# Optimization experiments

Hardware: AMD Instinct MI355X
Metric: run time of the kernel (lower is better)

## Reference

```python
import jax, jax.numpy as jnp
import numpy as np

EPS = 1e-08


def setup_inputs() -> dict:
    key = jax.random.key(0)
    x = jax.random.normal(key, (64, 16, 65536), dtype=jnp.float32)
    return {"x": x}


def reference(x):
    # x: (B, C, T). All statistics reduce over the last (time) axis.
    mean = x.mean(axis=-1)                       # (B, C)
    var = jnp.var(x, axis=-1, ddof=1)            # torch.var default: unbiased
    std = jnp.sqrt(var)                          # torch.std default: unbiased
    sq_mean = (x ** 2).mean(axis=-1)
    rms = jnp.sqrt(sq_mean)
    peak = x.max(axis=-1)
    peak_neg = x.min(axis=-1)
    peak_to_peak = peak - peak_neg
    abs_peak = jnp.abs(peak)
    crest_factor = abs_peak / (rms + EPS)
    mean_abs = jnp.abs(x).mean(axis=-1)
    shape_factor = rms / (mean_abs + EPS)
    impulse_factor = abs_peak / (mean_abs + EPS)
    sqrt_mean = jnp.sqrt(jnp.abs(x)).mean(axis=-1)
    clearance_factor = abs_peak / (sqrt_mean ** 2 + EPS)

    centered = x - mean[..., None]               # (B, C, T)
    skewness = (centered ** 3).mean(axis=-1) / (std ** 3 + EPS)
    kurtosis_val = (centered ** 4).mean(axis=-1) / (std ** 4 + EPS) - 3.0

    signs = jnp.sign(x)
    zcr = (signs[:, :, 1:] != signs[:, :, :-1]).astype(jnp.float32).mean(axis=-1)
    centered_signs = jnp.sign(centered)
    mcr = (centered_signs[:, :, 1:] != centered_signs[:, :, :-1]).astype(jnp.float32).mean(axis=-1)

    margin_factor = abs_peak / (sqrt_mean + EPS)
    energy = (x ** 2).sum(axis=-1)

    features = jnp.stack([
        mean, std, var, rms, peak, peak_neg, peak_to_peak,
        crest_factor, shape_factor, impulse_factor, clearance_factor,
        skewness, kurtosis_val, zcr, mcr, margin_factor, energy,
    ], axis=-1)                                  # (B, C, 17)
    return features
```

## Files before the change

### kernel.cpp

```cpp
#include <hip/hip_runtime.h>
#include <math.h>

#define T_LEN  65536
#define TPB    256
#define VECS   (T_LEN / 4)
#define VPT    (VECS / TPB)
#define NSUPER (VPT / 4)
#define NWAVES (TPB / 64)
#define NB     (VECS / 64)
#define EPS    1e-8f

#define BANDB  0.05f
#define WCAP   1536

struct Acc {
    float s1, s2, s3, s4, sa, ss, mx, mn;
    int mcb;
};

__device__ __forceinline__ int mbcnt64(unsigned long long m) {
    int c = __builtin_amdgcn_mbcnt_lo((unsigned)m, 0);
    return __builtin_amdgcn_mbcnt_hi((unsigned)(m >> 32), c);
}

__device__ __forceinline__ void pair_cls(float p, float q, Acc& a,
                                         float2* __restrict__ mycand, int& wcnt) {
    float lo = fminf(p, q), hi = fmaxf(p, q);
    bool always = (lo < -BANDB) && (hi >= BANDB);
    bool never  = (lo >= BANDB) || (hi < -BANDB);
    a.mcb += (int)always;
    bool st = !(always || never);
    unsigned long long mask = __ballot(st);
    if (st) {
        int o = wcnt + mbcnt64(mask);
        if (o < WCAP) mycand[o] = make_float2(lo, hi);
    }
    wcnt += __builtin_popcountll(mask);
}

__device__ __forceinline__ void p1_body(const float4& v, int lane, Acc& a,
                                        float2* __restrict__ mycand, int& wcnt) {
    float prev = __shfl_up(v.w, 1);
    if (lane == 0) prev = v.x;

    pair_cls(prev, v.x, a, mycand, wcnt);
    pair_cls(v.x, v.y, a, mycand, wcnt);
    pair_cls(v.y, v.z, a, mycand, wcnt);
    pair_cls(v.z, v.w, a, mycand, wcnt);

    float e0 = v.x, e1 = v.y, e2 = v.z, e3 = v.w;
    a.s1 += e0 + e1 + e2 + e3;
    a.s2 = fmaf(e0, e0, a.s2); a.s2 = fmaf(e1, e1, a.s2);
    a.s2 = fmaf(e2, e2, a.s2); a.s2 = fmaf(e3, e3, a.s2);
    a.s3 = fmaf(e0 * e0, e0, a.s3); a.s3 = fmaf(e1 * e1, e1, a.s3);
    a.s3 = fmaf(e2 * e2, e2, a.s3); a.s3 = fmaf(e3 * e3, e3, a.s3);
    a.s4 = fmaf(e0 * e0, e0 * e0, a.s4); a.s4 = fmaf(e1 * e1, e1 * e1, a.s4);
    a.s4 = fmaf(e2 * e2, e2 * e2, a.s4); a.s4 = fmaf(e3 * e3, e3 * e3, a.s4);
    float a0 = fabsf(e0), a1 = fabsf(e1), a2 = fabsf(e2), a3 = fabsf(e3);
    a.sa += a0 + a1 + a2 + a3;
    a.ss += __builtin_amdgcn_sqrtf(a0) + __builtin_amdgcn_sqrtf(a1)
          + __builtin_amdgcn_sqrtf(a2) + __builtin_amdgcn_sqrtf(a3);
    a.mx = fmaxf(fmaxf(a.mx, e0), fmaxf(e1, fmaxf(e2, e3)));
    a.mn = fminf(fminf(a.mn, e0), fminf(e1, fminf(e2, e3)));
}

__device__ __forceinline__ void p2f(const float4& v, int lane, float m,
                                    int& mc, int& zc) {
    float prev = __shfl_up(v.w, 1);
    if (lane == 0) prev = v.x;
    bool spm = prev < m, szp = prev < 0.f;
    bool m0 = v.x < m, m1 = v.y < m, m2 = v.z < m, m3 = v.w < m;
    bool z0 = v.x < 0.f, z1 = v.y < 0.f, z2 = v.z < 0.f, z3 = v.w < 0.f;
    mc += (int)(spm != m0) + (int)(m0 != m1) + (int)(m1 != m2) + (int)(m2 != m3);
    zc += (int)(szp != z0) + (int)(z0 != z1) + (int)(z1 != z2) + (int)(z2 != z3);
}

__global__ __launch_bounds__(TPB) void stat_feat_fused(const float* __restrict__ x,
                                                       float* __restrict__ out) {
    const int row  = blockIdx.x;
    const int tid  = threadIdx.x;
    const int lane = tid & 63;
    const int wave = tid >> 6;

    const float4* __restrict__ xv = (const float4*)(x + (size_t)row * T_LEN);

    __shared__ float  l[10][NWAVES];
    __shared__ float  s_mean;
    __shared__ float  wlast[NB];
    __shared__ float  xfirst[NB];
    __shared__ float2 cand[NWAVES * WCAP];
    __shared__ int    wc[NWAVES];

    float2* __restrict__ mycand = cand + wave * WCAP;
    int wcnt = 0;

    Acc a;
    a.s1 = a.s2 = a.s3 = a.s4 = a.sa = a.ss = 0.f;
    a.mx = -__builtin_inff();
    a.mn = __builtin_inff();
    a.mcb = 0;

    for (int g = 0; g < NSUPER; ++g) {
        const int base = g * 4 * TPB + tid;
        const int ia = base, ib = base + TPB, ic = base + 2 * TPB, id = base + 3 * TPB;
        float4 va = xv[ia];
        float4 vb = xv[ib];
        float4 vc = xv[ic];
        float4 vd = xv[id];
        if (lane == 63) {
            wlast[ia >> 6] = va.w; wlast[ib >> 6] = vb.w;
            wlast[ic >> 6] = vc.w; wlast[id >> 6] = vd.w;
        }
        if (lane == 0) {
            xfirst[ia >> 6] = va.x; xfirst[ib >> 6] = vb.x;
            xfirst[ic >> 6] = vc.x; xfirst[id >> 6] = vd.x;
        }
        p1_body(va, lane, a, mycand, wcnt);
        p1_body(vb, lane, a, mycand, wcnt);
        p1_body(vc, lane, a, mycand, wcnt);
        p1_body(vd, lane, a, mycand, wcnt);
    }

#pragma unroll
    for (int o = 32; o > 0; o >>= 1) {
        a.s1 += __shfl_down(a.s1, o);
        a.s2 += __shfl_down(a.s2, o);
        a.s3 += __shfl_down(a.s3, o);
        a.s4 += __shfl_down(a.s4, o);
        a.sa += __shfl_down(a.sa, o);
        a.ss += __shfl_down(a.ss, o);
        a.mcb += __shfl_down(a.mcb, o);
        a.mx = fmaxf(a.mx, __shfl_down(a.mx, o));
        a.mn = fminf(a.mn, __shfl_down(a.mn, o));
    }

    if (lane == 0) {
        l[0][wave] = a.s1; l[1][wave] = a.s2; l[2][wave] = a.s3; l[3][wave] = a.s4;
        l[4][wave] = a.sa; l[5][wave] = a.ss; l[6][wave] = a.mx; l[7][wave] = a.mn;
        l[8][wave] = (float)a.mcb;
        wc[wave] = wcnt;
    }
    __syncthreads();

    float S1 = 0.f, S2 = 0.f, S3 = 0.f, S4 = 0.f, SA = 0.f, SS = 0.f, MCB = 0.f;
    float MX = -__builtin_inff(), MN = __builtin_inff();
    if (tid == 0) {
#pragma unroll
        for (int wv = 0; wv < NWAVES; wv++) {
            S1 += l[0][wv]; S2 += l[1][wv]; S3 += l[2][wv]; S4 += l[3][wv];
            SA += l[4][wv]; SS += l[5][wv];
            MX = fmaxf(MX, l[6][wv]); MN = fminf(MN, l[7][wv]);
            MCB += l[8][wv];
        }
        s_mean = S1 / (float)T_LEN;
    }
    __syncthreads();

    const float m = s_mean;
    const bool fb = (fabsf(m) >= BANDB) | (wc[0] > WCAP) | (wc[1] > WCAP)
                  | (wc[2] > WCAP) | (wc[3] > WCAP);
    int mcc = 0, zcc = 0;
    if (!fb) {
#pragma unroll
        for (int w = 0; w < NWAVES; w++) {
            const int n = wc[w];
            const float2* __restrict__ cw = cand + w * WCAP;
            for (int i = tid; i < n; i += TPB) {
                float2 c = cw[i];
                mcc += (int)((c.x < m) && (c.y >= m));
                zcc += (int)((c.x < 0.f) && (c.y >= 0.f));
            }
        }
    } else {
        for (int g = 0; g < NSUPER; ++g) {
            const int base = g * 4 * TPB + tid;
            const int ia = base, ib = base + TPB, ic = base + 2 * TPB, id = base + 3 * TPB;
            float4 va = xv[ia];
            float4 vb = xv[ib];
            float4 vc = xv[ic];
            float4 vd = xv[id];
            p2f(va, lane, m, mcc, zcc);
            p2f(vb, lane, m, mcc, zcc);
            p2f(vc, lane, m, mcc, zcc);
            p2f(vd, lane, m, mcc, zcc);
        }
    }

    int mb = 0, zb = 0;
    if (tid > 0) {
        float wl = wlast[tid - 1];
        float xf = xfirst[tid];
        zb = (int)((wl < 0.f) != (xf < 0.f));
        mb = (int)((wl < m) != (xf < m));
    }

#pragma unroll
    for (int o = 32; o > 0; o >>= 1) {
        mcc += __shfl_down(mcc, o);
        zcc += __shfl_down(zcc, o);
        mb  += __shfl_down(mb, o);
        zb  += __shfl_down(zb, o);
    }

    __syncthreads();
    if (lane == 0) {
        l[0][wave] = (float)mcc;
        l[1][wave] = (float)zcc;
        l[2][wave] = (float)mb;
        l[3][wave] = (float)zb;
    }
    __syncthreads();

    if (tid == 0) {
        float MC = 0.f, ZCC = 0.f, MB = 0.f, ZB = 0.f;
#pragma unroll
        for (int wv = 0; wv < NWAVES; wv++) {
            MC += l[0][wv]; ZCC += l[1][wv]; MB += l[2][wv]; ZB += l[3][wv];
        }
        float ZC;
        if (!fb) {
            MC += MCB + MB;
            ZC  = ZCC + MCB + ZB;
        } else {
            MC += MB;
            ZC  = ZCC + ZB;
        }

        const float Tf = (float)T_LEN;
        float mean = S1 / Tf;
        float sq_mean = S2 / Tf;
        float var = (S2 - S1 * S1 / Tf) / (Tf - 1.f);
        var = fmaxf(var, 0.f);
        float stdv = sqrtf(var);
        float rms = sqrtf(sq_mean);
        float peak = MX, peak_neg = MN;
        float ptp = peak - peak_neg;
        float abs_peak = fabsf(peak);
        float crest = abs_peak / (rms + EPS);
        float mean_abs = SA / Tf;
        float shape = rms / (mean_abs + EPS);
        float impulse = abs_peak / (mean_abs + EPS);
        float sqrt_mean = SS / Tf;
        float clearance = abs_peak / (sqrt_mean * sqrt_mean + EPS);
        float ex3 = S3 / Tf;
        float m3 = ex3 - 3.f * mean * sq_mean + 2.f * mean * mean * mean;
        float m4 = S4 / Tf - 4.f * mean * ex3 + 6.f * mean * mean * sq_mean
                   - 3.f * mean * mean * mean * mean;
        float skew = m3 / (stdv * stdv * stdv + EPS);
        float kurt = m4 / (stdv * stdv * stdv * stdv + EPS) - 3.f;
        float zcr = ZC / (Tf - 1.f);
        float mcr = MC / (Tf - 1.f);
        float margin = abs_peak / (sqrt_mean + EPS);

        float* o = out + (size_t)row * 17;
        o[0] = mean;   o[1] = stdv;     o[2] = var;        o[3] = rms;
        o[4] = peak;   o[5] = peak_neg; o[6] = ptp;        o[7] = crest;
        o[8] = shape;  o[9] = impulse;  o[10] = clearance; o[11] = skew;
        o[12] = kurt;  o[13] = zcr;     o[14] = mcr;       o[15] = margin;
        o[16] = S2;
    }
}

extern "C" void kernel_launch(void* const* d_in, const int* in_sizes, int n_in,
                              void* d_out, int out_size, void* d_ws, size_t ws_size,
                              hipStream_t stream) {
    const float* x = (const float*)d_in[0];
    float* out = (float*)d_out;
    const int rows = in_sizes[0] / T_LEN;
    stat_feat_fused<<<dim3(rows), dim3(TPB), 0, stream>>>(x, out);
}
```

Measured before the change: 381.1 us.

## Prefetch next tile, branchless candidate stores, narrower band, wave-level crossing counts

Register double-buffers the next four float4 loads so global reads overlap the compute of the current group. It also makes candidate stores branchless by sending non-candidates to a per-lane dump slot, and classifies each element once instead of once per pair. Crossing counts for guaranteed sign changes now come from a ballot popcount per wave. The band narrows to 0.025 with a smaller per-wave capacity, which cuts LDS use and may raise occupancy, but overflow into the full second pass over global memory becomes more likely.

```diff
diff --git a/kernel.cpp b/kernel.cpp
--- a/kernel.cpp
+++ b/kernel.cpp
@@ -10,43 +10,45 @@
 #define NB     (VECS / 64)
 #define EPS    1e-8f
 
-#define BANDB  0.05f
-#define WCAP   1536
-
-struct Acc {
-    float s1, s2, s3, s4, sa, ss, mx, mn;
-    int mcb;
-};
+#define BANDB  0.025f
+#define WCAP   832
+#define DUMPO  (NWAVES * WCAP)
+
+struct Acc { float s1, s2, s3, s4, sa, ss, mx, mn; };
 
 __device__ __forceinline__ int mbcnt64(unsigned long long m) {
     int c = __builtin_amdgcn_mbcnt_lo((unsigned)m, 0);
     return __builtin_amdgcn_mbcnt_hi((unsigned)(m >> 32), c);
 }
 
-__device__ __forceinline__ void pair_cls(float p, float q, Acc& a,
-                                         float2* __restrict__ mycand, int& wcnt) {
-    float lo = fminf(p, q), hi = fmaxf(p, q);
-    bool always = (lo < -BANDB) && (hi >= BANDB);
-    bool never  = (lo >= BANDB) || (hi < -BANDB);
-    a.mcb += (int)always;
-    bool st = !(always || never);
+__device__ __forceinline__ void pair_one(float p, float q,
+                                         bool pbel, bool pabv, bool pinb,
+                                         bool qbel, bool qabv, bool qinb,
+                                         float2* __restrict__ cand, int wbase,
+                                         int dumpidx, int& wcnt, int& wmcb) {
+    bool always = (pbel & qabv) | (pabv & qbel);
+    wmcb += __builtin_popcountll(__ballot(always));
+    bool st = pinb | qinb;
     unsigned long long mask = __ballot(st);
-    if (st) {
-        int o = wcnt + mbcnt64(mask);
-        if (o < WCAP) mycand[o] = make_float2(lo, hi);
-    }
+    int o = wcnt + mbcnt64(mask);
+    int idx = (st && (o < WCAP)) ? (wbase + o) : dumpidx;
+    cand[idx] = make_float2(fminf(p, q), fmaxf(p, q));
     wcnt += __builtin_popcountll(mask);
 }
 
-__device__ __forceinline__ void p1_body(const float4& v, int lane, Acc& a,
-                                        float2* __restrict__ mycand, int& wcnt) {
-    float prev = __shfl_up(v.w, 1);
-    if (lane == 0) prev = v.x;
-
-    pair_cls(prev, v.x, a, mycand, wcnt);
-    pair_cls(v.x, v.y, a, mycand, wcnt);
-    pair_cls(v.y, v.z, a, mycand, wcnt);
-    pair_cls(v.z, v.w, a, mycand, wcnt);
+__device__ __forceinline__ void p1_body(const float4& v, float prev, Acc& a,
+                                        float2* __restrict__ cand, int wbase,
+                                        int dumpidx, int& wcnt, int& wmcb) {
+    bool pb = prev < -BANDB, pa = prev >= BANDB, pi = !(pb | pa);
+    bool b0 = v.x < -BANDB, a0 = v.x >= BANDB, i0 = !(b0 | a0);
+    bool b1 = v.y < -BANDB, a1 = v.y >= BANDB, i1 = !(b1 | a1);
+    bool b2 = v.z < -BANDB, a2 = v.z >= BANDB, i2 = !(b2 | a2);
+    bool b3 = v.w < -BANDB, a3 = v.w >= BANDB, i3 = !(b3 | a3);
+
+    pair_one(prev, v.x, pb, pa, pi, b0, a0, i0, cand, wbase, dumpidx, wcnt, wmcb);
+    pair_one(v.x, v.y, b0, a0, i0, b1, a1, i1, cand, wbase, dumpidx, wcnt, wmcb);
+    pair_one(v.y, v.z, b1, a1, i1, b2, a2, i2, cand, wbase, dumpidx, wcnt, wmcb);
+    pair_one(v.z, v.w, b2, a2, i2, b3, a3, i3, cand, wbase, dumpidx, wcnt, wmcb);
 
     float e0 = v.x, e1 = v.y, e2 = v.z, e3 = v.w;
     a.s1 += e0 + e1 + e2 + e3;
@@ -56,10 +58,10 @@
     a.s3 = fmaf(e2 * e2, e2, a.s3); a.s3 = fmaf(e3 * e3, e3, a.s3);
     a.s4 = fmaf(e0 * e0, e0 * e0, a.s4); a.s4 = fmaf(e1 * e1, e1 * e1, a.s4);
     a.s4 = fmaf(e2 * e2, e2 * e2, a.s4); a.s4 = fmaf(e3 * e3, e3 * e3, a.s4);
-    float a0 = fabsf(e0), a1 = fabsf(e1), a2 = fabsf(e2), a3 = fabsf(e3);
-    a.sa += a0 + a1 + a2 + a3;
-    a.ss += __builtin_amdgcn_sqrtf(a0) + __builtin_amdgcn_sqrtf(a1)
-          + __builtin_amdgcn_sqrtf(a2) + __builtin_amdgcn_sqrtf(a3);
+    float a0f = fabsf(e0), a1f = fabsf(e1), a2f = fabsf(e2), a3f = fabsf(e3);
+    a.sa += a0f + a1f + a2f + a3f;
+    a.ss += __builtin_amdgcn_sqrtf(a0f) + __builtin_amdgcn_sqrtf(a1f)
+          + __builtin_amdgcn_sqrtf(a2f) + __builtin_amdgcn_sqrtf(a3f);
     a.mx = fmaxf(fmaxf(a.mx, e0), fmaxf(e1, fmaxf(e2, e3)));
     a.mn = fminf(fminf(a.mn, e0), fminf(e1, fminf(e2, e3)));
 }
@@ -88,37 +90,51 @@
     __shared__ float  s_mean;
     __shared__ float  wlast[NB];
     __shared__ float  xfirst[NB];
-    __shared__ float2 cand[NWAVES * WCAP];
+    __shared__ float2 cand[DUMPO + NWAVES * 64];
     __shared__ int    wc[NWAVES];
 
-    float2* __restrict__ mycand = cand + wave * WCAP;
+    const int wbase   = wave * WCAP;
+    const int dumpidx = DUMPO + wave * 64 + lane;
     int wcnt = 0;
+    int wmcb = 0;
 
     Acc a;
     a.s1 = a.s2 = a.s3 = a.s4 = a.sa = a.ss = 0.f;
     a.mx = -__builtin_inff();
     a.mn = __builtin_inff();
-    a.mcb = 0;
+
+    float4 c0 = xv[tid], c1 = xv[tid + TPB], c2 = xv[tid + 2 * TPB],
+           c3 = xv[tid + 3 * TPB];
 
     for (int g = 0; g < NSUPER; ++g) {
-        const int base = g * 4 * TPB + tid;
-        const int ia = base, ib = base + TPB, ic = base + 2 * TPB, id = base + 3 * TPB;
-        float4 va = xv[ia];
-        float4 vb = xv[ib];
-        float4 vc = xv[ic];
-        float4 vd = xv[id];
+        const int gn = (g + 1 < NSUPER) ? g + 1 : g;
+        const int nbs = gn * 4 * TPB + tid;
+        float4 n0 = xv[nbs], n1 = xv[nbs + TPB], n2 = xv[nbs + 2 * TPB],
+               n3 = xv[nbs + 3 * TPB];
+
+        const int ia = g * 4 * TPB + tid, ib = ia + TPB,
+                  ic = ia + 2 * TPB, id = ia + 3 * TPB;
         if (lane == 63) {
-            wlast[ia >> 6] = va.w; wlast[ib >> 6] = vb.w;
-            wlast[ic >> 6] = vc.w; wlast[id >> 6] = vd.w;
+            wlast[ia >> 6] = c0.w; wlast[ib >> 6] = c1.w;
+            wlast[ic >> 6] = c2.w; wlast[id >> 6] = c3.w;
         }
         if (lane == 0) {
-            xfirst[ia >> 6] = va.x; xfirst[ib >> 6] = vb.x;
-            xfirst[ic >> 6] = vc.x; xfirst[id >> 6] = vd.x;
-        }
-        p1_body(va, lane, a, mycand, wcnt);
-        p1_body(vb, lane, a, mycand, wcnt);
-        p1_body(vc, lane, a, mycand, wcnt);
-        p1_body(vd, lane, a, mycand, wcnt);
+            xfirst[ia >> 6] = c0.x; xfirst[ib >> 6] = c1.x;
+            xfirst[ic >> 6] = c2.x; xfirst[id >> 6] = c3.x;
+        }
+
+        float p0 = __shfl_up(c0.w, 1);
+        float p1 = __shfl_up(c1.w, 1);
+        float p2 = __shfl_up(c2.w, 1);
+        float p3 = __shfl_up(c3.w, 1);
+        if (lane == 0) { p0 = c0.x; p1 = c1.x; p2 = c2.x; p3 = c3.x; }
+
+        p1_body(c0, p0, a, cand, wbase, dumpidx, wcnt, wmcb);
+        p1_body(c1, p1, a, cand, wbase, dumpidx, wcnt, wmcb);
+        p1_body(c2, p2, a, cand, wbase, dumpidx, wcnt, wmcb);
+        p1_body(c3, p3, a, cand, wbase, dumpidx, wcnt, wmcb);
+
+        c0 = n0; c1 = n1; c2 = n2; c3 = n3;
     }
 
 #pragma unroll
@@ -129,7 +145,6 @@
         a.s4 += __shfl_down(a.s4, o);
         a.sa += __shfl_down(a.sa, o);
         a.ss += __shfl_down(a.ss, o);
-        a.mcb += __shfl_down(a.mcb, o);
         a.mx = fmaxf(a.mx, __shfl_down(a.mx, o));
         a.mn = fminf(a.mn, __shfl_down(a.mn, o));
     }
@@ -137,7 +152,7 @@
     if (lane == 0) {
         l[0][wave] = a.s1; l[1][wave] = a.s2; l[2][wave] = a.s3; l[3][wave] = a.s4;
         l[4][wave] = a.sa; l[5][wave] = a.ss; l[6][wave] = a.mx; l[7][wave] = a.mn;
-        l[8][wave] = (float)a.mcb;
+        l[8][wave] = (float)wmcb;
         wc[wave] = wcnt;
     }
     __syncthreads();
@@ -174,11 +189,10 @@
     } else {
         for (int g = 0; g < NSUPER; ++g) {
             const int base = g * 4 * TPB + tid;
-            const int ia = base, ib = base + TPB, ic = base + 2 * TPB, id = base + 3 * TPB;
-            float4 va = xv[ia];
-            float4 vb = xv[ib];
-            float4 vc = xv[ic];
-            float4 vd = xv[id];
+            float4 va = xv[base];
+            float4 vb = xv[base + TPB];
+            float4 vc = xv[base + 2 * TPB];
+            float4 vd = xv[base + 3 * TPB];
             p2f(va, lane, m, mcc, zcc);
             p2f(vb, lane, m, mcc, zcc);
             p2f(vc, lane, m, mcc, zcc);
```

Result: faster. 366.0 us (-4.0%).
